# Kernel tuning notes

Measured on AMD Instinct MI355X. Metric: run time of the kernel, lower is better.

## Reference

```python
import jax, jax.numpy as jnp
import numpy as np


def setup_inputs() -> dict:
    key = jax.random.key(0)
    ks = jax.random.split(key, 7)
    B, P, D = 4, 2048, 1024
    s = 1.0 / np.sqrt(D)
    return {
        "x":  jax.random.normal(ks[0], (B, P, D), dtype=jnp.float32),
        "Wq": jax.random.normal(ks[1], (D, D), dtype=jnp.float32) * s,
        "bq": jnp.zeros((D,), dtype=jnp.float32),
        "Wk": jax.random.normal(ks[2], (D, D), dtype=jnp.float32) * s,
        "bk": jnp.zeros((D,), dtype=jnp.float32),
        "Wv": jax.random.normal(ks[3], (D, D), dtype=jnp.float32) * s,
        "bv": jnp.zeros((D,), dtype=jnp.float32),
    }


def reference(x, Wq, bq, Wk, bk, Wv, bv):
    # x: [B, P, D]; Linear uses W stored torch-style [out, in]: y = x @ W.T + b
    b, p, d = x.shape
    q = jnp.einsum("bpd,ed->bpe", x, Wq) + bq
    k = jnp.einsum("bpd,ed->bpe", x, Wk) + bk
    v = jnp.einsum("bpd,ed->bpe", x, Wv) + bv
    attn = jnp.einsum("bqd,bkd->bqk", q, k)  # [B, P, P]
    causal = jnp.triu(jnp.ones((p, p), dtype=bool), k=1)  # True above diagonal
    attn = jnp.where(causal, -jnp.inf, attn)
    attn = attn / jnp.sqrt(jnp.asarray(d, dtype=attn.dtype))
    scores = jax.nn.softmax(attn, axis=-1)
    # dropout is identity in eval/deterministic mode
    return jnp.einsum("bqk,bkd->bqd", scores, v)
```

## Files before the change

kernel.cpp:

```cpp
#include <hip/hip_runtime.h>
#include <hip/hip_bf16.h>


typedef __attribute__((ext_vector_type(8))) short bf16x8;
typedef __attribute__((ext_vector_type(4))) float f32x4;

__device__ __forceinline__ unsigned short f2bf(float f) {
    union { float f; unsigned u; } v; v.f = f;
    unsigned r = v.u + 0x7FFF + ((v.u >> 16) & 1);
    return (unsigned short)(r >> 16);
}

__device__ __forceinline__ void gload_lds16(const unsigned short* g, unsigned short* l) {
    __builtin_amdgcn_global_load_lds(
        (const __attribute__((address_space(1))) unsigned int*)g,
        (__attribute__((address_space(3))) unsigned int*)l, 16, 0, 0);
}

__global__ void convert_kernel(const float* __restrict__ x,  const float* __restrict__ wq,
                               const float* __restrict__ wk, const float* __restrict__ wv,
                               const float* __restrict__ bq, const float* __restrict__ bk,
                               const float* __restrict__ bv,
                               unsigned short* __restrict__ xb, unsigned short* __restrict__ wqkvb,
                               float* __restrict__ bqkv, float* __restrict__ lsum) {
    long t = (long)blockIdx.x * blockDim.x + threadIdx.x;
    long idx = t * 4;
    const float* src; unsigned short* dst; long off;
    if      (idx <  8388608) { src = x;  dst = xb;            off = idx;            }
    else if (idx <  9437184) { src = wq; dst = wqkvb;         off = idx -  8388608; }
    else if (idx < 10485760) { src = wk; dst = wqkvb+1048576; off = idx -  9437184; }
    else if (idx < 11534336) { src = wv; dst = wqkvb+2097152; off = idx - 10485760; }
    else return;
    float4 v = *(const float4*)(src + off);
    ushort4 o = make_ushort4(f2bf(v.x), f2bf(v.y), f2bf(v.z), f2bf(v.w));
    *(ushort4*)(dst + off) = o;
    if (t < 768) {
        long o2 = t * 4;
        float4 b;
        if      (o2 < 1024) b = *(const float4*)(bq + o2);
        else if (o2 < 2048) b = *(const float4*)(bk + o2 - 1024);
        else                b = *(const float4*)(bv + o2 - 2048);
        *(float4*)(bqkv + o2) = b;
    }
    if (t >= 1024 && t < 3072) {
        float4 z = make_float4(0.f, 0.f, 0.f, 0.f);
        *(float4*)(lsum + (t - 1024) * 4) = z;
    }
}

__global__ void transpose_v(const unsigned short* __restrict__ V,
                            unsigned short* __restrict__ VT) {
    __shared__ unsigned short t[64][72];
    const int p0 = blockIdx.x * 64;
    const int e0 = blockIdx.y * 64;
    const int r = threadIdx.x >> 3;
    const int c = (threadIdx.x & 7) * 8;
    const unsigned short* src = V + (long)(p0 + r) * 3072 + e0 + c;
    *(int4*)&t[r][c]      = *(const int4*)src;
    *(int4*)&t[r + 32][c] = *(const int4*)(src + 32 * 3072);
    __syncthreads();
    unsigned short ov[8];
    unsigned short* dst = VT + (long)(e0 + r) * 8192 + p0 + c;
#pragma unroll
    for (int j = 0; j < 8; ++j) ov[j] = t[c + j][r];
    *(int4*)dst = *(int4*)ov;
    dst = VT + (long)(e0 + r + 32) * 8192 + p0 + c;
#pragma unroll
    for (int j = 0; j < 8; ++j) ov[j] = t[c + j][r + 32];
    *(int4*)dst = *(int4*)ov;
}

template<int MODE>
__global__ void gemm_bt(const unsigned short* __restrict__ A, int lda,
                        const unsigned short* __restrict__ B, int ldb,
                        unsigned short* __restrict__ Cb, float* __restrict__ Cf, int ldc,
                        const float* __restrict__ bias_col, float* __restrict__ lsum,
                        int K, long bsA, long bsB, long bsC, long bsL) {
    const int n0 = blockIdx.x * 128;
    const int m0 = blockIdx.y * 128;
    if (MODE == 1 && n0 > m0) return;
    const int z = blockIdx.z;
    A += (long)z * bsA;
    B += (long)z * bsB;
    if (MODE == 2) Cf += (long)z * bsC; else Cb += (long)z * bsC;
    if (MODE != 0) lsum += (long)z * bsL;

    const int Keff = (MODE == 2) ? (m0 + 128) : K;

    __shared__ unsigned short As[128 * 32];
    __shared__ unsigned short Bs[128 * 32];

    const int tid  = threadIdx.x;
    const int lane = tid & 63;
    const int w    = tid >> 6;
    const int wr   = (w >> 1) * 64;
    const int wc   = (w & 1) * 64;
    const int q    = lane >> 4;
    const int ln   = lane & 15;

    const int l4 = lane >> 2;
    const int lc = (lane & 3) ^ (l4 & 3);
    const unsigned short* gA  = A + (long)(m0 + w * 32 + l4) * lda + lc * 8;
    const unsigned short* gA2 = gA + (long)16 * lda;
    const unsigned short* gB  = B + (long)(n0 + w * 32 + l4) * ldb + lc * 8;
    const unsigned short* gB2 = gB + (long)16 * ldb;
    unsigned short* lA  = &As[(w * 32) * 32];
    unsigned short* lA2 = &As[(w * 32 + 16) * 32];
    unsigned short* lB  = &Bs[(w * 32) * 32];
    unsigned short* lB2 = &Bs[(w * 32 + 16) * 32];

    const int pos = (q ^ (ln & 3)) * 8;

    f32x4 acc[4][4] = {};

    for (int k0 = 0; k0 < Keff; k0 += 32) {
        __syncthreads();
        gload_lds16(gA + k0, lA);
        gload_lds16(gA2 + k0, lA2);
        gload_lds16(gB + k0, lB);
        gload_lds16(gB2 + k0, lB2);
        __syncthreads();
        bf16x8 af[4], bfr[4];
#pragma unroll
        for (int i = 0; i < 4; ++i)
            af[i] = *(const bf16x8*)(&As[(wr + i * 16 + ln) * 32 + pos]);
#pragma unroll
        for (int j = 0; j < 4; ++j)
            bfr[j] = *(const bf16x8*)(&Bs[(wc + j * 16 + ln) * 32 + pos]);
#pragma unroll
        for (int i = 0; i < 4; ++i)
#pragma unroll
            for (int j = 0; j < 4; ++j)
                acc[i][j] = __builtin_amdgcn_mfma_f32_16x16x32_bf16(af[i], bfr[j], acc[i][j], 0, 0, 0);
    }

    if (MODE == 0) {
#pragma unroll
        for (int i = 0; i < 4; ++i) {
            const int rowb = m0 + wr + i * 16 + q * 4;
#pragma unroll
            for (int r = 0; r < 4; ++r) {
                const int row = rowb + r;
#pragma unroll
                for (int j = 0; j < 4; ++j) {
                    const int col = n0 + wc + j * 16 + ln;
                    Cb[(long)row * ldc + col] = f2bf(acc[i][j][r] + bias_col[col]);
                }
            }
        }
    } else if (MODE == 1) {
        const float scale = 0.03125f;
#pragma unroll
        for (int i = 0; i < 4; ++i) {
            float rsum[4] = {0.f, 0.f, 0.f, 0.f};
#pragma unroll
            for (int r = 0; r < 4; ++r) {
                const int row = m0 + wr + i * 16 + q * 4 + r;
#pragma unroll
                for (int j = 0; j < 4; ++j) {
                    const int col = n0 + wc + j * 16 + ln;
                    float p = (col <= row) ? __expf(acc[i][j][r] * scale) : 0.f;
                    rsum[r] += p;
                    Cb[(long)row * ldc + col] = f2bf(p);
                }
            }
#pragma unroll
            for (int r = 0; r < 4; ++r) {
                float s = rsum[r];
                s += __shfl_xor(s, 1); s += __shfl_xor(s, 2);
                s += __shfl_xor(s, 4); s += __shfl_xor(s, 8);
                if (ln == 0) atomicAdd(&lsum[m0 + wr + i * 16 + q * 4 + r], s);
            }
        }
    } else {
#pragma unroll
        for (int i = 0; i < 4; ++i) {
#pragma unroll
            for (int r = 0; r < 4; ++r) {
                const int row = m0 + wr + i * 16 + q * 4 + r;
                const float inv = 1.0f / lsum[row];
#pragma unroll
                for (int j = 0; j < 4; ++j) {
                    const int col = n0 + wc + j * 16 + ln;
                    Cf[(long)row * ldc + col] = acc[i][j][r] * inv;
                }
            }
        }
    }
}

extern "C" void kernel_launch(void* const* d_in, const int* in_sizes, int n_in,
                              void* d_out, int out_size, void* d_ws, size_t ws_size,
                              hipStream_t stream) {
    const float* x  = (const float*)d_in[0];
    const float* Wq = (const float*)d_in[1];
    const float* bq = (const float*)d_in[2];
    const float* Wk = (const float*)d_in[3];
    const float* bk = (const float*)d_in[4];
    const float* Wv = (const float*)d_in[5];
    const float* bv = (const float*)d_in[6];
    float* out = (float*)d_out;

    char* ws = (char*)d_ws;
    unsigned short* xb    = (unsigned short*)ws;
    unsigned short* VTb   = (unsigned short*)ws;
    ws += (long)8192 * 1024 * 2;
    unsigned short* wqkvb = (unsigned short*)ws; ws += (long)3072 * 1024 * 2;
    float*          bqkv  = (float*)ws;          ws += (long)3072 * 4;
    float*          lsum  = (float*)ws;          ws += (long)8192 * 4;
    unsigned short* QKVb  = (unsigned short*)ws; ws += (long)8192 * 3072 * 2;
    unsigned short* Pb    = (unsigned short*)ws; ws += (long)4 * 2048 * 2048 * 2;

    hipLaunchKernelGGL(convert_kernel, dim3(11264), dim3(256), 0, stream,
                       x, Wq, Wk, Wv, bq, bk, bv, xb, wqkvb, bqkv, lsum);

    hipLaunchKernelGGL((gemm_bt<0>), dim3(24, 64, 1), dim3(256), 0, stream,
                       xb, 1024, wqkvb, 1024, QKVb, (float*)nullptr, 3072,
                       bqkv, (float*)nullptr, 1024, 0L, 0L, 0L, 0L);

    hipLaunchKernelGGL(transpose_v, dim3(128, 16, 1), dim3(256), 0, stream,
                       QKVb + 2048, VTb);

    hipLaunchKernelGGL((gemm_bt<1>), dim3(16, 16, 4), dim3(256), 0, stream,
                       QKVb, 3072, QKVb + 1024, 3072, Pb, (float*)nullptr, 2048,
                       (const float*)nullptr, lsum,
                       1024, (long)2048 * 3072, (long)2048 * 3072, (long)2048 * 2048, 2048L);

    hipLaunchKernelGGL((gemm_bt<2>), dim3(8, 16, 4), dim3(256), 0, stream,
                       Pb, 2048, VTb, 8192, (unsigned short*)nullptr, out, 1024,
                       (const float*)nullptr, lsum,
                       2048, (long)2048 * 2048, 2048L, (long)2048 * 1024, 2048L);
}
```

Baseline: 269.0 us.

## Use 2-wave 128x128 GEMM blocks with K=64 tiles and swapped MFMA operands

The shared GEMM kernel goes from 4 waves of 64x64 warp tiles to 2 waves, each computing a 64x128 tile, with the K step doubled to 64 and an XOR swizzle widened to 8 chunks. MFMA operands are swapped so each lane holds 4 consecutive columns, which allows vectorized ushort4/float4 stores and a simpler row-sum reduction with fewer atomics. The intent is more MFMA work per LDS load, fewer barriers per K, and wider global stores. The cost is higher register pressure from 32 accumulators per lane, and fewer waves per block may weaken latency hiding.

```diff
diff --git a/kernel.cpp b/kernel.cpp
--- a/kernel.cpp
+++ b/kernel.cpp
@@ -71,11 +71,12 @@
 }
 
 template<int MODE>
-__global__ void gemm_bt(const unsigned short* __restrict__ A, int lda,
-                        const unsigned short* __restrict__ B, int ldb,
-                        unsigned short* __restrict__ Cb, float* __restrict__ Cf, int ldc,
-                        const float* __restrict__ bias_col, float* __restrict__ lsum,
-                        int K, long bsA, long bsB, long bsC, long bsL) {
+__global__ __launch_bounds__(128, 2)
+void gemm_bt(const unsigned short* __restrict__ A, int lda,
+             const unsigned short* __restrict__ B, int ldb,
+             unsigned short* __restrict__ Cb, float* __restrict__ Cf, int ldc,
+             const float* __restrict__ bias_col, float* __restrict__ lsum,
+             int K, long bsA, long bsB, long bsC, long bsL) {
     const int n0 = blockIdx.x * 128;
     const int m0 = blockIdx.y * 128;
     if (MODE == 1 && n0 > m0) return;
@@ -87,103 +88,101 @@
 
     const int Keff = (MODE == 2) ? (m0 + 128) : K;
 
-    __shared__ unsigned short As[128 * 32];
-    __shared__ unsigned short Bs[128 * 32];
+    __shared__ unsigned short As[128 * 64];
+    __shared__ unsigned short Bs[128 * 64];
 
     const int tid  = threadIdx.x;
     const int lane = tid & 63;
     const int w    = tid >> 6;
-    const int wr   = (w >> 1) * 64;
-    const int wc   = (w & 1) * 64;
     const int q    = lane >> 4;
     const int ln   = lane & 15;
 
-    const int l4 = lane >> 2;
-    const int lc = (lane & 3) ^ (l4 & 3);
-    const unsigned short* gA  = A + (long)(m0 + w * 32 + l4) * lda + lc * 8;
-    const unsigned short* gA2 = gA + (long)16 * lda;
-    const unsigned short* gB  = B + (long)(n0 + w * 32 + l4) * ldb + lc * 8;
-    const unsigned short* gB2 = gB + (long)16 * ldb;
-    unsigned short* lA  = &As[(w * 32) * 32];
-    unsigned short* lA2 = &As[(w * 32 + 16) * 32];
-    unsigned short* lB  = &Bs[(w * 32) * 32];
-    unsigned short* lB2 = &Bs[(w * 32 + 16) * 32];
-
-    const int pos = (q ^ (ln & 3)) * 8;
-
-    f32x4 acc[4][4] = {};
-
-    for (int k0 = 0; k0 < Keff; k0 += 32) {
+    const int srow = lane >> 3;
+    const int sc   = (lane & 7) ^ (srow & 7);
+    const unsigned short* gA = A + (long)(m0 + w * 64 + srow) * lda + sc * 8;
+    const unsigned short* gB = B + (long)(n0 + w * 64 + srow) * ldb + sc * 8;
+    unsigned short* lA = &As[(w * 64) * 64];
+    unsigned short* lB = &Bs[(w * 64) * 64];
+
+    const int pr0 = ((q)     ^ (ln & 7)) * 8;
+    const int pr1 = ((q + 4) ^ (ln & 7)) * 8;
+
+    f32x4 acc[4][8] = {};
+
+    for (int k0 = 0; k0 < Keff; k0 += 64) {
         __syncthreads();
-        gload_lds16(gA + k0, lA);
-        gload_lds16(gA2 + k0, lA2);
-        gload_lds16(gB + k0, lB);
-        gload_lds16(gB2 + k0, lB2);
+#pragma unroll
+        for (int s = 0; s < 8; ++s) {
+            gload_lds16(gA + k0 + (long)(s * 8) * lda, lA + (s * 8) * 64);
+            gload_lds16(gB + k0 + (long)(s * 8) * ldb, lB + (s * 8) * 64);
+        }
         __syncthreads();
-        bf16x8 af[4], bfr[4];
-#pragma unroll
-        for (int i = 0; i < 4; ++i)
-            af[i] = *(const bf16x8*)(&As[(wr + i * 16 + ln) * 32 + pos]);
-#pragma unroll
-        for (int j = 0; j < 4; ++j)
-            bfr[j] = *(const bf16x8*)(&Bs[(wc + j * 16 + ln) * 32 + pos]);
-#pragma unroll
-        for (int i = 0; i < 4; ++i)
-#pragma unroll
-            for (int j = 0; j < 4; ++j)
-                acc[i][j] = __builtin_amdgcn_mfma_f32_16x16x32_bf16(af[i], bfr[j], acc[i][j], 0, 0, 0);
+#pragma unroll
+        for (int kk = 0; kk < 2; ++kk) {
+            const int pr = kk ? pr1 : pr0;
+            bf16x8 af[4], bfr[8];
+#pragma unroll
+            for (int i = 0; i < 4; ++i)
+                af[i] = *(const bf16x8*)(&As[(w * 64 + i * 16 + ln) * 64 + pr]);
+#pragma unroll
+            for (int j = 0; j < 8; ++j)
+                bfr[j] = *(const bf16x8*)(&Bs[(j * 16 + ln) * 64 + pr]);
+#pragma unroll
+            for (int i = 0; i < 4; ++i)
+#pragma unroll
+                for (int j = 0; j < 8; ++j)
+                    acc[i][j] = __builtin_amdgcn_mfma_f32_16x16x32_bf16(bfr[j], af[i], acc[i][j], 0, 0, 0);
+        }
     }
 
     if (MODE == 0) {
 #pragma unroll
-        for (int i = 0; i < 4; ++i) {
-            const int rowb = m0 + wr + i * 16 + q * 4;
-#pragma unroll
-            for (int r = 0; r < 4; ++r) {
-                const int row = rowb + r;
-#pragma unroll
-                for (int j = 0; j < 4; ++j) {
-                    const int col = n0 + wc + j * 16 + ln;
-                    Cb[(long)row * ldc + col] = f2bf(acc[i][j][r] + bias_col[col]);
-                }
+        for (int j = 0; j < 8; ++j) {
+            const float4 bc = *(const float4*)(bias_col + n0 + j * 16 + q * 4);
+#pragma unroll
+            for (int i = 0; i < 4; ++i) {
+                const int m = m0 + w * 64 + i * 16 + ln;
+                const int n = n0 + j * 16 + q * 4;
+                ushort4 o = make_ushort4(f2bf(acc[i][j][0] + bc.x), f2bf(acc[i][j][1] + bc.y),
+                                         f2bf(acc[i][j][2] + bc.z), f2bf(acc[i][j][3] + bc.w));
+                *(ushort4*)(Cb + (long)m * ldc + n) = o;
             }
         }
     } else if (MODE == 1) {
         const float scale = 0.03125f;
+        float rs[4] = {0.f, 0.f, 0.f, 0.f};
 #pragma unroll
         for (int i = 0; i < 4; ++i) {
-            float rsum[4] = {0.f, 0.f, 0.f, 0.f};
-#pragma unroll
-            for (int r = 0; r < 4; ++r) {
-                const int row = m0 + wr + i * 16 + q * 4 + r;
-#pragma unroll
-                for (int j = 0; j < 4; ++j) {
-                    const int col = n0 + wc + j * 16 + ln;
-                    float p = (col <= row) ? __expf(acc[i][j][r] * scale) : 0.f;
-                    rsum[r] += p;
-                    Cb[(long)row * ldc + col] = f2bf(p);
-                }
+            const int m = m0 + w * 64 + i * 16 + ln;
+#pragma unroll
+            for (int j = 0; j < 8; ++j) {
+                const int n = n0 + j * 16 + q * 4;
+                float p0 = (n     <= m) ? __expf(acc[i][j][0] * scale) : 0.f;
+                float p1 = (n + 1 <= m) ? __expf(acc[i][j][1] * scale) : 0.f;
+                float p2 = (n + 2 <= m) ? __expf(acc[i][j][2] * scale) : 0.f;
+                float p3 = (n + 3 <= m) ? __expf(acc[i][j][3] * scale) : 0.f;
+                rs[i] += (p0 + p1) + (p2 + p3);
+                ushort4 o = make_ushort4(f2bf(p0), f2bf(p1), f2bf(p2), f2bf(p3));
+                *(ushort4*)(Cb + (long)m * ldc + n) = o;
             }
-#pragma unroll
-            for (int r = 0; r < 4; ++r) {
-                float s = rsum[r];
-                s += __shfl_xor(s, 1); s += __shfl_xor(s, 2);
-                s += __shfl_xor(s, 4); s += __shfl_xor(s, 8);
-                if (ln == 0) atomicAdd(&lsum[m0 + wr + i * 16 + q * 4 + r], s);
-            }
+        }
+#pragma unroll
+        for (int i = 0; i < 4; ++i) {
+            float s = rs[i];
+            s += __shfl_xor(s, 16); s += __shfl_xor(s, 32);
+            if (lane < 16) atomicAdd(&lsum[m0 + w * 64 + i * 16 + ln], s);
         }
     } else {
 #pragma unroll
         for (int i = 0; i < 4; ++i) {
-#pragma unroll
-            for (int r = 0; r < 4; ++r) {
-                const int row = m0 + wr + i * 16 + q * 4 + r;
-                const float inv = 1.0f / lsum[row];
-#pragma unroll
-                for (int j = 0; j < 4; ++j) {
-                    const int col = n0 + wc + j * 16 + ln;
-                    Cf[(long)row * ldc + col] = acc[i][j][r] * inv;
-                }
+            const int m = m0 + w * 64 + i * 16 + ln;
+            const float inv = 1.0f / lsum[m];
+#pragma unroll
+            for (int j = 0; j < 8; ++j) {
+                const int n = n0 + j * 16 + q * 4;
+                float4 o = make_float4(acc[i][j][0] * inv, acc[i][j][1] * inv,
+                                       acc[i][j][2] * inv, acc[i][j][3] * inv);
+                *(float4*)(Cf + (long)m * ldc + n) = o;
             }
         }
     }
@@ -214,19 +213,19 @@
     hipLaunchKernelGGL(convert_kernel, dim3(11264), dim3(256), 0, stream,
                        x, Wq, Wk, Wv, bq, bk, bv, xb, wqkvb, bqkv, lsum);
 
-    hipLaunchKernelGGL((gemm_bt<0>), dim3(24, 64, 1), dim3(256), 0, stream,
+    hipLaunchKernelGGL((gemm_bt<0>), dim3(24, 64, 1), dim3(128), 0, stream,
                        xb, 1024, wqkvb, 1024, QKVb, (float*)nullptr, 3072,
                        bqkv, (float*)nullptr, 1024, 0L, 0L, 0L, 0L);
 
     hipLaunchKernelGGL(transpose_v, dim3(128, 16, 1), dim3(256), 0, stream,
                        QKVb + 2048, VTb);
 
-    hipLaunchKernelGGL((gemm_bt<1>), dim3(16, 16, 4), dim3(256), 0, stream,
+    hipLaunchKernelGGL((gemm_bt<1>), dim3(16, 16, 4), dim3(128), 0, stream,
                        QKVb, 3072, QKVb + 1024, 3072, Pb, (float*)nullptr, 2048,
                        (const float*)nullptr, lsum,
                        1024, (long)2048 * 3072, (long)2048 * 3072, (long)2048 * 2048, 2048L);
 
-    hipLaunchKernelGGL((gemm_bt<2>), dim3(8, 16, 4), dim3(256), 0, stream,
+    hipLaunchKernelGGL((gemm_bt<2>), dim3(8, 16, 4), dim3(128), 0, stream,
                        Pb, 2048, VTb, 8192, (unsigned short*)nullptr, out, 1024,
                        (const float*)nullptr, lsum,
                        2048, (long)2048 * 2048, 2048L, (long)2048 * 1024, 2048L);
```

Result: no change. 266.4 us (-1.0%).
